# Kernel tuning notes

Measured on AMD Instinct MI355X. Metric: run time of the kernel, lower is better.

Reference implementation:

```python
import jax, jax.numpy as jnp
import numpy as np

N_NODES = 100000
N_EDGES = 3200000
N_GRAPHS = 64
IN_DIM, OUT_DIM = 16, 3


def _gcn_layer(x, src, dst, ew, W, b, n):
    # PyG GCNConv with edge_weight: transform first, then normalized propagate
    # with added self-loops (weight 1.0). deg_i = sum_{e: dst=i} w_e + 1.
    xw = x @ W  # [N, out]
    deg = jax.ops.segment_sum(ew, dst, num_segments=n) + 1.0  # [N]
    dinv = jax.lax.rsqrt(deg)
    norm = dinv[src] * ew * dinv[dst]  # [E]
    agg = jax.ops.segment_sum(xw[src] * norm[:, None], dst, num_segments=n)
    # self-loop contribution: dinv_i * 1.0 * dinv_i = 1/deg_i
    return agg + xw * (1.0 / deg)[:, None] + b


def setup_inputs() -> dict:
    key = jax.random.key(0)
    ks = jax.random.split(key, 16)
    glorot = lambda k, fi, fo: jax.random.normal(k, (fi, fo), jnp.float32) * jnp.sqrt(2.0 / (fi + fo))
    return {
        "x": jax.random.normal(ks[0], (N_NODES, IN_DIM), jnp.float32),
        "edge_index": jax.random.randint(ks[1], (2, N_EDGES), 0, N_NODES, jnp.int32),
        "edge_attr": jax.random.uniform(ks[2], (N_EDGES,), jnp.float32),
        "batch": jnp.sort(jax.random.randint(ks[3], (N_NODES,), 0, N_GRAPHS, jnp.int32)),
        "W1": glorot(ks[4], IN_DIM, 16), "b1": jnp.zeros((16,), jnp.float32),
        "W2": glorot(ks[5], 16, 64),     "b2": jnp.zeros((64,), jnp.float32),
        "W3": glorot(ks[6], 64, 256),    "b3": jnp.zeros((256,), jnp.float32),
        "L1": glorot(ks[7], 256, 128),   "c1": jnp.zeros((128,), jnp.float32),
        "L2": glorot(ks[8], 128, 64),    "c2": jnp.zeros((64,), jnp.float32),
        "L3": glorot(ks[9], 64, OUT_DIM), "c3": jnp.zeros((OUT_DIM,), jnp.float32),
    }


def reference(x, edge_index, edge_attr, batch, W1, b1, W2, b2, W3, b3, L1, c1, L2, c2, L3, c3):
    src, dst = edge_index[0], edge_index[1]
    h = jax.nn.silu(_gcn_layer(x, src, dst, edge_attr, W1, b1, N_NODES))
    h = jax.nn.silu(_gcn_layer(h, src, dst, edge_attr, W2, b2, N_NODES))
    h = jax.nn.silu(_gcn_layer(h, src, dst, edge_attr, W3, b3, N_NODES))
    # global mean pool per graph
    sums = jax.ops.segment_sum(h, batch, num_segments=N_GRAPHS)  # [G, 256]
    cnt = jax.ops.segment_sum(jnp.ones((N_NODES,), h.dtype), batch, num_segments=N_GRAPHS)
    pooled = sums / jnp.maximum(cnt, 1.0)[:, None]
    z = jax.nn.silu(pooled @ L1 + c1)
    z = jax.nn.silu(z @ L2 + c2)
    z = z @ L3 + c3
    return jnp.squeeze(z)
```

## Files before the change

kernel.cpp:

```cpp
#include <hip/hip_runtime.h>
#include <math.h>


#define NBH 256
#define POOL_C 8
#define X3T 32
#define CAP 10240

typedef _Float16 half8 __attribute__((ext_vector_type(8)));

__device__ __forceinline__ float silu_f(float v) { return v / (1.0f + expf(-v)); }
__device__ __forceinline__ void fma4(float4& a, float s, const float4& w) {
    a.x += s * w.x; a.y += s * w.y; a.z += s * w.z; a.w += s * w.w;
}

__global__ void k_init(const int* __restrict__ batch, int* __restrict__ bounds,
                       int* __restrict__ btotal, int N, int G) {
    int t = threadIdx.x;
    btotal[t] = 0;
    if (t > G) return;
    if (t == G) { bounds[G] = N; return; }
    int lo = 0, hi = N;
    while (lo < hi) { int m = (lo + hi) >> 1; if (batch[m] < t) lo = m + 1; else hi = m; }
    bounds[t] = lo;
}

__global__ __launch_bounds__(256) void k_bscatter(const int* __restrict__ src,
                                                  const int* __restrict__ dst,
                                                  const float* __restrict__ ew,
                                                  int* __restrict__ btotal,
                                                  int2* __restrict__ ebuf,
                                                  int E, int B, int ept) {
    __shared__ int hist[512];
    __shared__ int cur[512];
    int blk = blockIdx.x, t = threadIdx.x;
    for (int i = t; i < B; i += 256) hist[i] = 0;
    __syncthreads();
    int start = blk * 256 * ept;
    for (int j = 0; j < ept; j++) {
        int e = start + j * 256 + t;
        if (e < E) atomicAdd(&hist[dst[e] >> 8], 1);
    }
    __syncthreads();
    for (int b = t; b < B; b += 256)
        cur[b] = b * CAP + atomicAdd(&btotal[b], hist[b]);
    __syncthreads();
    for (int j = 0; j < ept; j++) {
        int e = start + j * 256 + t;
        if (e < E) {
            int d = dst[e];
            int b = d >> 8;
            int pos = atomicAdd(&cur[b], 1);
            if (pos < (b + 1) * CAP)
                ebuf[pos] = make_int2(src[e] | ((d & 255) << 24), __float_as_int(ew[e]));
        }
    }
}

__global__ __launch_bounds__(256) void k_bucket_csr(const int2* __restrict__ ebuf,
                                                    const int* __restrict__ btotal,
                                                    int2* __restrict__ csr,
                                                    unsigned int* __restrict__ offs,
                                                    float* __restrict__ dinv,
                                                    const float* __restrict__ x,
                                                    _Float16* __restrict__ xp,
                                                    int N) {
    __shared__ int ncnt[256];
    __shared__ int excl[256];
    __shared__ float wsum[256];
    int b = blockIdx.x, t = threadIdx.x;
    int base = b * CAP;
    int end = base + min(btotal[b], CAP);
    ncnt[t] = 0;
    wsum[t] = 0.0f;
    __syncthreads();
    for (int i = base + t; i < end; i += 256)
        atomicAdd(&ncnt[(unsigned)ebuf[i].x >> 24], 1);
    __syncthreads();
    int v = ncnt[t];
    excl[t] = v;
    __syncthreads();
#pragma unroll
    for (int o = 1; o < 256; o <<= 1) {
        int x2 = (t >= o) ? excl[t - o] : 0;
        __syncthreads();
        excl[t] += x2;
        __syncthreads();
    }
    int ex = excl[t] - v;
    int n = (b << 8) + t;
    if (n < N) offs[n] = (unsigned)(base + ex) | ((unsigned)v << 24);
    __syncthreads();
    ncnt[t] = base + ex;
    __syncthreads();
    for (int i = base + t; i < end; i += 256) {
        int2 ent = ebuf[i];
        int node = (unsigned)ent.x >> 24;
        int pos = atomicAdd(&ncnt[node], 1);
        csr[pos] = make_int2(ent.x & 0x00FFFFFF, ent.y);
        atomicAdd(&wsum[node], __int_as_float(ent.y));
    }
    __syncthreads();
    if (n < N) {
        float dv = 1.0f / sqrtf(1.0f + wsum[t]);
        dinv[n] = dv;
        const float4* xr = (const float4*)(x + (long long)n * 16);
        half8* xw = (half8*)(xp + (long long)n * 16);
#pragma unroll
        for (int j = 0; j < 2; j++) {
            float4 a = xr[2 * j], c = xr[2 * j + 1];
            half8 hv;
            hv[0] = (_Float16)(a.x * dv); hv[1] = (_Float16)(a.y * dv);
            hv[2] = (_Float16)(a.z * dv); hv[3] = (_Float16)(a.w * dv);
            hv[4] = (_Float16)(c.x * dv); hv[5] = (_Float16)(c.y * dv);
            hv[6] = (_Float16)(c.z * dv); hv[7] = (_Float16)(c.w * dv);
            xw[j] = hv;
        }
    }
}

__global__ __launch_bounds__(256) void k_gx1(const _Float16* __restrict__ h,
                                             const int2* __restrict__ csr,
                                             const unsigned int* __restrict__ offs,
                                             const float* __restrict__ dinv,
                                             const float* __restrict__ W,
                                             const float* __restrict__ b,
                                             _Float16* __restrict__ out, int N) {
    __shared__ float Ws[16 * 16];
    __shared__ float bs[16];
    if (threadIdx.x < 256) Ws[threadIdx.x] = W[threadIdx.x];
    if (threadIdx.x < 16) bs[threadIdx.x] = b[threadIdx.x];
    __syncthreads();
    int n = blockIdx.x * 4 + (threadIdx.x >> 6);
    n = __builtin_amdgcn_readfirstlane(n);
    if (n >= N) return;
    int lane = threadIdx.x & 63;
    int d = lane & 15, eg = lane >> 4;
    unsigned op = offs[n];
    int p0 = op & 0x00FFFFFF;
    int len = op >> 24;
    int qs = p0 + ((len * eg) >> 2);
    int qe = p0 + ((len * (eg + 1)) >> 2);
    float acc = 0.0f;
    int p = qs;
    for (; p + 7 < qe; p += 8) {
        int2 e0 = csr[p], e1 = csr[p + 1], e2 = csr[p + 2], e3 = csr[p + 3];
        int2 e4 = csr[p + 4], e5 = csr[p + 5], e6 = csr[p + 6], e7 = csr[p + 7];
        float v0 = (float)h[e0.x * 16 + d], v1 = (float)h[e1.x * 16 + d];
        float v2 = (float)h[e2.x * 16 + d], v3 = (float)h[e3.x * 16 + d];
        float v4 = (float)h[e4.x * 16 + d], v5 = (float)h[e5.x * 16 + d];
        float v6 = (float)h[e6.x * 16 + d], v7 = (float)h[e7.x * 16 + d];
        acc += __int_as_float(e0.y) * v0; acc += __int_as_float(e1.y) * v1;
        acc += __int_as_float(e2.y) * v2; acc += __int_as_float(e3.y) * v3;
        acc += __int_as_float(e4.y) * v4; acc += __int_as_float(e5.y) * v5;
        acc += __int_as_float(e6.y) * v6; acc += __int_as_float(e7.y) * v7;
    }
    if (p + 3 < qe) {
        int2 e0 = csr[p], e1 = csr[p + 1], e2 = csr[p + 2], e3 = csr[p + 3];
        float v0 = (float)h[e0.x * 16 + d], v1 = (float)h[e1.x * 16 + d];
        float v2 = (float)h[e2.x * 16 + d], v3 = (float)h[e3.x * 16 + d];
        acc += __int_as_float(e0.y) * v0; acc += __int_as_float(e1.y) * v1;
        acc += __int_as_float(e2.y) * v2; acc += __int_as_float(e3.y) * v3;
        p += 4;
    }
    if (p + 1 < qe) {
        int2 e0 = csr[p], e1 = csr[p + 1];
        acc += __int_as_float(e0.y) * (float)h[e0.x * 16 + d];
        acc += __int_as_float(e1.y) * (float)h[e1.x * 16 + d];
        p += 2;
    }
    if (p < qe) {
        int2 e0 = csr[p];
        acc += __int_as_float(e0.y) * (float)h[e0.x * 16 + d];
    }
    acc += __shfl_down(acc, 32, 64);
    acc += __shfl_down(acc, 16, 64);
    float dv = dinv[n];
    float yv = (acc + ((lane < 16) ? (float)h[n * 16 + lane] : 0.0f)) * dv;
    float o = bs[d];
#pragma unroll
    for (int k = 0; k < 16; k++) o += __shfl(yv, k, 64) * Ws[k * 16 + d];
    if (lane < 16) out[n * 16 + lane] = (_Float16)(silu_f(o) * dv);
}

__global__ __launch_bounds__(256) void k_gx2(const _Float16* __restrict__ h,
                                             const int2* __restrict__ csr,
                                             const unsigned int* __restrict__ offs,
                                             const float* __restrict__ dinv,
                                             const float* __restrict__ W,
                                             const float* __restrict__ b,
                                             _Float16* __restrict__ out, int N) {
    __shared__ float Ws[16 * 64];
    __shared__ float bs[64];
    for (int i = threadIdx.x; i < 16 * 64; i += 256) Ws[i] = W[i];
    if (threadIdx.x < 64) bs[threadIdx.x] = b[threadIdx.x];
    __syncthreads();
    int n = blockIdx.x * 4 + (threadIdx.x >> 6);
    n = __builtin_amdgcn_readfirstlane(n);
    if (n >= N) return;
    int lane = threadIdx.x & 63;
    int d = lane & 15, eg = lane >> 4;
    unsigned op = offs[n];
    int p0 = op & 0x00FFFFFF;
    int len = op >> 24;
    int qs = p0 + ((len * eg) >> 2);
    int qe = p0 + ((len * (eg + 1)) >> 2);
    float acc = 0.0f;
    int p = qs;
    for (; p + 7 < qe; p += 8) {
        int2 e0 = csr[p], e1 = csr[p + 1], e2 = csr[p + 2], e3 = csr[p + 3];
        int2 e4 = csr[p + 4], e5 = csr[p + 5], e6 = csr[p + 6], e7 = csr[p + 7];
        float v0 = (float)h[e0.x * 16 + d], v1 = (float)h[e1.x * 16 + d];
        float v2 = (float)h[e2.x * 16 + d], v3 = (float)h[e3.x * 16 + d];
        float v4 = (float)h[e4.x * 16 + d], v5 = (float)h[e5.x * 16 + d];
        float v6 = (float)h[e6.x * 16 + d], v7 = (float)h[e7.x * 16 + d];
        acc += __int_as_float(e0.y) * v0; acc += __int_as_float(e1.y) * v1;
        acc += __int_as_float(e2.y) * v2; acc += __int_as_float(e3.y) * v3;
        acc += __int_as_float(e4.y) * v4; acc += __int_as_float(e5.y) * v5;
        acc += __int_as_float(e6.y) * v6; acc += __int_as_float(e7.y) * v7;
    }
    if (p + 3 < qe) {
        int2 e0 = csr[p], e1 = csr[p + 1], e2 = csr[p + 2], e3 = csr[p + 3];
        float v0 = (float)h[e0.x * 16 + d], v1 = (float)h[e1.x * 16 + d];
        float v2 = (float)h[e2.x * 16 + d], v3 = (float)h[e3.x * 16 + d];
        acc += __int_as_float(e0.y) * v0; acc += __int_as_float(e1.y) * v1;
        acc += __int_as_float(e2.y) * v2; acc += __int_as_float(e3.y) * v3;
        p += 4;
    }
    if (p + 1 < qe) {
        int2 e0 = csr[p], e1 = csr[p + 1];
        acc += __int_as_float(e0.y) * (float)h[e0.x * 16 + d];
        acc += __int_as_float(e1.y) * (float)h[e1.x * 16 + d];
        p += 2;
    }
    if (p < qe) {
        int2 e0 = csr[p];
        acc += __int_as_float(e0.y) * (float)h[e0.x * 16 + d];
    }
    acc += __shfl_down(acc, 32, 64);
    acc += __shfl_down(acc, 16, 64);
    float dv = dinv[n];
    float yv = (acc + ((lane < 16) ? (float)h[n * 16 + lane] : 0.0f)) * dv;
    float o = bs[lane];
#pragma unroll
    for (int k = 0; k < 16; k++) o += __shfl(yv, k, 64) * Ws[k * 64 + lane];
    out[(long long)n * 64 + lane] = (_Float16)(silu_f(o) * dv);
}

__global__ __launch_bounds__(256) void k_gather64(const _Float16* __restrict__ h,
                                                  const int2* __restrict__ csr,
                                                  const unsigned int* __restrict__ offs,
                                                  const float* __restrict__ dinv,
                                                  float* __restrict__ y, int N) {
    int n = blockIdx.x * 4 + (threadIdx.x >> 6);
    n = __builtin_amdgcn_readfirstlane(n);
    if (n >= N) return;
    int lane = threadIdx.x & 63;
    unsigned op = offs[n];
    const int2* row = csr + (op & 0x00FFFFFF);
    int len = op >> 24;
    float acc = 0.0f;
    int j = 0;
    for (; j + 7 < len; j += 8) {
        int2 ee[8];
        float vv[8];
#pragma unroll
        for (int i = 0; i < 8; i++) ee[i] = row[j + i];
#pragma unroll
        for (int i = 0; i < 8; i++) vv[i] = (float)h[ee[i].x * 64 + lane];
#pragma unroll
        for (int i = 0; i < 8; i++) acc += __int_as_float(ee[i].y) * vv[i];
    }
    if (j + 3 < len) {
        int2 e0 = row[j], e1 = row[j + 1], e2 = row[j + 2], e3 = row[j + 3];
        float v0 = (float)h[e0.x * 64 + lane];
        float v1 = (float)h[e1.x * 64 + lane];
        float v2 = (float)h[e2.x * 64 + lane];
        float v3 = (float)h[e3.x * 64 + lane];
        acc += __int_as_float(e0.y) * v0;
        acc += __int_as_float(e1.y) * v1;
        acc += __int_as_float(e2.y) * v2;
        acc += __int_as_float(e3.y) * v3;
        j += 4;
    }
    for (; j < len; j++) {
        int2 e0 = row[j];
        acc += __int_as_float(e0.y) * (float)h[e0.x * 64 + lane];
    }
    y[n * 64 + lane] = (acc + (float)h[n * 64 + lane]) * dinv[n];
}

__global__ __launch_bounds__(256) void k_xform3pool(const float* __restrict__ y,
                                                    const float* __restrict__ W,
                                                    const float* __restrict__ b,
                                                    const int* __restrict__ bounds,
                                                    float* __restrict__ partial) {
    __shared__ float4 Ws[64 * 64];
    __shared__ float4 ys4[X3T * 16];
    __shared__ float4 red[3][64];
    for (int i = threadIdx.x; i < 64 * 64; i += 256) Ws[i] = ((const float4*)W)[i];
    int lane = threadIdx.x & 63;
    int wave = threadIdx.x >> 6;
    int g = blockIdx.x / POOL_C;
    int c = blockIdx.x % POOL_C;
    int s = bounds[g], e = bounds[g + 1];
    int len = e - s;
    int cs = s + (int)((long long)len * c / POOL_C);
    int ce = s + (int)((long long)len * (c + 1) / POOL_C);
    float4 bv = ((const float4*)b)[lane];
    float4 pacc = make_float4(0.f, 0.f, 0.f, 0.f);
    int nb = wave * 8;
    for (int base = cs; base < ce; base += X3T) {
        int tcnt = min(X3T, ce - base);
        __syncthreads();
        {
            const float4* ysrc = (const float4*)(y + (long long)base * 64);
            for (int i = threadIdx.x; i < tcnt * 16; i += 256) ys4[i] = ysrc[i];
        }
        __syncthreads();
        float4 acc[8];
#pragma unroll
        for (int i = 0; i < 8; i++) acc[i] = bv;
#pragma unroll 2
        for (int kq = 0; kq < 16; kq++) {
            float4 w0 = Ws[(4 * kq + 0) * 64 + lane];
            float4 w1 = Ws[(4 * kq + 1) * 64 + lane];
            float4 w2 = Ws[(4 * kq + 2) * 64 + lane];
            float4 w3 = Ws[(4 * kq + 3) * 64 + lane];
#pragma unroll
            for (int i = 0; i < 8; i++) {
                float4 yv = ys4[(nb + i) * 16 + kq];
                fma4(acc[i], yv.x, w0); fma4(acc[i], yv.y, w1);
                fma4(acc[i], yv.z, w2); fma4(acc[i], yv.w, w3);
            }
        }
#pragma unroll
        for (int i = 0; i < 8; i++) {
            if (base + nb + i < ce) {
                pacc.x += silu_f(acc[i].x); pacc.y += silu_f(acc[i].y);
                pacc.z += silu_f(acc[i].z); pacc.w += silu_f(acc[i].w);
            }
        }
    }
    __syncthreads();
    if (wave > 0) red[wave - 1][lane] = pacc;
    __syncthreads();
    if (wave == 0) {
        float4 r0 = red[0][lane], r1 = red[1][lane], r2 = red[2][lane];
        pacc.x += r0.x + r1.x + r2.x;
        pacc.y += r0.y + r1.y + r2.y;
        pacc.z += r0.z + r1.z + r2.z;
        pacc.w += r0.w + r1.w + r2.w;
        ((float4*)partial)[(long long)blockIdx.x * 64 + lane] = pacc;
    }
}

__global__ __launch_bounds__(256) void k_mlp(const float* __restrict__ partial,
                                             const int* __restrict__ bounds,
                                             const float* __restrict__ L1,
                                             const float* __restrict__ c1,
                                             const float* __restrict__ L2,
                                             const float* __restrict__ c2,
                                             const float* __restrict__ L3,
                                             const float* __restrict__ c3,
                                             float* __restrict__ out) {
    __shared__ float pooled[256];
    __shared__ float z1[128];
    __shared__ float z2[64];
    int g = blockIdx.x;
    int t = threadIdx.x;
    int cnt = bounds[g + 1] - bounds[g];
    float s = 0.0f;
    for (int c = 0; c < POOL_C; c++) s += partial[((long long)g * POOL_C + c) * 256 + t];
    pooled[t] = s / (float)(cnt > 0 ? cnt : 1);
    __syncthreads();
    if (t < 128) {
        float acc = c1[t];
        for (int k = 0; k < 256; k++) acc += pooled[k] * L1[k * 128 + t];
        z1[t] = silu_f(acc);
    }
    __syncthreads();
    if (t < 64) {
        float acc = c2[t];
        for (int k = 0; k < 128; k++) acc += z1[k] * L2[k * 64 + t];
        z2[t] = silu_f(acc);
    }
    __syncthreads();
    if (t < 3) {
        float acc = c3[t];
        for (int k = 0; k < 64; k++) acc += z2[k] * L3[k * 3 + t];
        out[g * 3 + t] = acc;
    }
}

extern "C" void kernel_launch(void* const* d_in, const int* in_sizes, int n_in,
                              void* d_out, int out_size, void* d_ws, size_t ws_size,
                              hipStream_t stream) {
    const float* x     = (const float*)d_in[0];
    const int*   ei    = (const int*)d_in[1];
    const float* ea    = (const float*)d_in[2];
    const int*   batch = (const int*)d_in[3];
    const float* W1 = (const float*)d_in[4];
    const float* b1 = (const float*)d_in[5];
    const float* W2 = (const float*)d_in[6];
    const float* b2 = (const float*)d_in[7];
    const float* W3 = (const float*)d_in[8];
    const float* b3 = (const float*)d_in[9];
    const float* L1 = (const float*)d_in[10];
    const float* c1 = (const float*)d_in[11];
    const float* L2 = (const float*)d_in[12];
    const float* c2 = (const float*)d_in[13];
    const float* L3 = (const float*)d_in[14];
    const float* c3 = (const float*)d_in[15];
    float* out = (float*)d_out;

    const int N = in_sizes[0] / 16;
    const int E = in_sizes[2];
    const int G = out_size / 3;
    const int* src = ei;
    const int* dst = ei + E;
    const int B = (N + 255) >> 8;
    const int ept = (E + NBH * 256 - 1) / (NBH * 256);

    char* ws = (char*)d_ws;
    size_t off = 0;
    auto alloc = [&](size_t bytes) -> void* {
        void* p = (void*)(ws + off);
        off += (bytes + 255) & ~(size_t)255;
        return p;
    };
    float*        dinv    = (float*)alloc((size_t)N * 4);
    unsigned int* offs    = (unsigned int*)alloc((size_t)N * 4);
    int*          btotal  = (int*)  alloc(512 * 4);
    int*          bounds  = (int*)  alloc((size_t)(G + 1) * 4);
    int2*         ebuf    = (int2*) alloc((size_t)B * CAP * 8);
    int2*         csr     = (int2*) alloc((size_t)B * CAP * 8);
    _Float16*     xp      = (_Float16*)alloc((size_t)N * 16 * 2);
    _Float16*     h1s     = (_Float16*)alloc((size_t)N * 16 * 2);
    _Float16*     h2s     = (_Float16*)alloc((size_t)N * 64 * 2);
    float*        y64     = (float*)alloc((size_t)N * 64 * 4);
    float*        partial = (float*)alloc((size_t)G * POOL_C * 256 * 4);
    (void)ws_size;

    k_init<<<1, 512, 0, stream>>>(batch, bounds, btotal, N, G);
    k_bscatter<<<NBH, 256, 0, stream>>>(src, dst, ea, btotal, ebuf, E, B, ept);
    k_bucket_csr<<<B, 256, 0, stream>>>(ebuf, btotal, csr, offs, dinv, x, xp, N);

    k_gx1<<<(N + 3) / 4, 256, 0, stream>>>(xp, csr, offs, dinv, W1, b1, h1s, N);

    k_gx2<<<(N + 3) / 4, 256, 0, stream>>>(h1s, csr, offs, dinv, W2, b2, h2s, N);

    k_gather64<<<(N + 3) / 4, 256, 0, stream>>>(h2s, csr, offs, dinv, y64, N);
    k_xform3pool<<<G * POOL_C, 256, 0, stream>>>(y64, W3, b3, bounds, partial);

    k_mlp<<<G, 256, 0, stream>>>(partial, bounds, L1, c1, L2, c2, L3, c3, out);
}
```

Before: 477.3 us.

## Use FP16 MFMA for layer-3 transform and pool, store y64 in half

```diff
diff --git a/kernel.cpp b/kernel.cpp
--- a/kernel.cpp
+++ b/kernel.cpp
@@ -4,15 +4,12 @@
 
 #define NBH 256
 #define POOL_C 8
-#define X3T 32
 #define CAP 10240
 
 typedef _Float16 half8 __attribute__((ext_vector_type(8)));
+typedef float f32x4 __attribute__((ext_vector_type(4)));
 
 __device__ __forceinline__ float silu_f(float v) { return v / (1.0f + expf(-v)); }
-__device__ __forceinline__ void fma4(float4& a, float s, const float4& w) {
-    a.x += s * w.x; a.y += s * w.y; a.z += s * w.z; a.w += s * w.w;
-}
 
 __global__ void k_init(const int* __restrict__ batch, int* __restrict__ bounds,
                        int* __restrict__ btotal, int N, int G) {
@@ -23,6 +20,12 @@
     int lo = 0, hi = N;
     while (lo < hi) { int m = (lo + hi) >> 1; if (batch[m] < t) lo = m + 1; else hi = m; }
     bounds[t] = lo;
+}
+
+__global__ __launch_bounds__(256) void k_cvtW3(const float* __restrict__ W,
+                                               _Float16* __restrict__ Wh, int n) {
+    int i = blockIdx.x * 256 + threadIdx.x;
+    if (i < n) Wh[i] = (_Float16)W[i];
 }
 
 __global__ __launch_bounds__(256) void k_bscatter(const int* __restrict__ src,
@@ -251,7 +254,7 @@
                                                   const int2* __restrict__ csr,
                                                   const unsigned int* __restrict__ offs,
                                                   const float* __restrict__ dinv,
-                                                  float* __restrict__ y, int N) {
+                                                  _Float16* __restrict__ y, int N) {
     int n = blockIdx.x * 4 + (threadIdx.x >> 6);
     n = __builtin_amdgcn_readfirstlane(n);
     if (n >= N) return;
@@ -287,18 +290,15 @@
         int2 e0 = row[j];
         acc += __int_as_float(e0.y) * (float)h[e0.x * 64 + lane];
     }
-    y[n * 64 + lane] = (acc + (float)h[n * 64 + lane]) * dinv[n];
-}
-
-__global__ __launch_bounds__(256) void k_xform3pool(const float* __restrict__ y,
-                                                    const float* __restrict__ W,
+    y[n * 64 + lane] = (_Float16)((acc + (float)h[n * 64 + lane]) * dinv[n]);
+}
+
+__global__ __launch_bounds__(256) void k_xform3pool(const _Float16* __restrict__ y,
+                                                    const _Float16* __restrict__ Wh,
                                                     const float* __restrict__ b,
                                                     const int* __restrict__ bounds,
-                                                    float* __restrict__ partial) {
-    __shared__ float4 Ws[64 * 64];
-    __shared__ float4 ys4[X3T * 16];
-    __shared__ float4 red[3][64];
-    for (int i = threadIdx.x; i < 64 * 64; i += 256) Ws[i] = ((const float4*)W)[i];
+                                                    float* __restrict__ partial,
+                                                    int N) {
     int lane = threadIdx.x & 63;
     int wave = threadIdx.x >> 6;
     int g = blockIdx.x / POOL_C;
@@ -307,51 +307,55 @@
     int len = e - s;
     int cs = s + (int)((long long)len * c / POOL_C);
     int ce = s + (int)((long long)len * (c + 1) / POOL_C);
-    float4 bv = ((const float4*)b)[lane];
-    float4 pacc = make_float4(0.f, 0.f, 0.f, 0.f);
-    int nb = wave * 8;
-    for (int base = cs; base < ce; base += X3T) {
-        int tcnt = min(X3T, ce - base);
-        __syncthreads();
-        {
-            const float4* ysrc = (const float4*)(y + (long long)base * 64);
-            for (int i = threadIdx.x; i < tcnt * 16; i += 256) ys4[i] = ysrc[i];
+    int lg = lane >> 4;
+    int lr = lane & 15;
+
+    half8 bf[4][2];
+#pragma unroll
+    for (int t = 0; t < 4; t++) {
+        int col = (wave * 4 + t) * 16 + lr;
+#pragma unroll
+        for (int s2 = 0; s2 < 2; s2++) {
+            half8 v;
+#pragma unroll
+            for (int j = 0; j < 8; j++)
+                v[j] = Wh[(s2 * 32 + lg * 8 + j) * 256 + col];
+            bf[t][s2] = v;
         }
-        __syncthreads();
-        float4 acc[8];
-#pragma unroll
-        for (int i = 0; i < 8; i++) acc[i] = bv;
-#pragma unroll 2
-        for (int kq = 0; kq < 16; kq++) {
-            float4 w0 = Ws[(4 * kq + 0) * 64 + lane];
-            float4 w1 = Ws[(4 * kq + 1) * 64 + lane];
-            float4 w2 = Ws[(4 * kq + 2) * 64 + lane];
-            float4 w3 = Ws[(4 * kq + 3) * 64 + lane];
-#pragma unroll
-            for (int i = 0; i < 8; i++) {
-                float4 yv = ys4[(nb + i) * 16 + kq];
-                fma4(acc[i], yv.x, w0); fma4(acc[i], yv.y, w1);
-                fma4(acc[i], yv.z, w2); fma4(acc[i], yv.w, w3);
+    }
+    float bias[4];
+#pragma unroll
+    for (int t = 0; t < 4; t++) bias[t] = b[(wave * 4 + t) * 16 + lr];
+
+    float pacc[4] = {0.f, 0.f, 0.f, 0.f};
+
+    for (int base = cs; base < ce; base += 16) {
+        int node = base + lr;
+        int cn = node < N ? node : N - 1;
+        const half8* arow = (const half8*)(y + (long long)cn * 64);
+        half8 a0 = arow[lg];
+        half8 a1 = arow[4 + lg];
+#pragma unroll
+        for (int t = 0; t < 4; t++) {
+            f32x4 acc = {0.f, 0.f, 0.f, 0.f};
+            acc = __builtin_amdgcn_mfma_f32_16x16x32_f16(a0, bf[t][0], acc, 0, 0, 0);
+            acc = __builtin_amdgcn_mfma_f32_16x16x32_f16(a1, bf[t][1], acc, 0, 0, 0);
+#pragma unroll
+            for (int r = 0; r < 4; r++) {
+                int nrow = base + lg * 4 + r;
+                if (nrow < ce) pacc[t] += silu_f(acc[r] + bias[t]);
             }
         }
-#pragma unroll
-        for (int i = 0; i < 8; i++) {
-            if (base + nb + i < ce) {
-                pacc.x += silu_f(acc[i].x); pacc.y += silu_f(acc[i].y);
-                pacc.z += silu_f(acc[i].z); pacc.w += silu_f(acc[i].w);
-            }
-        }
-    }
-    __syncthreads();
-    if (wave > 0) red[wave - 1][lane] = pacc;
-    __syncthreads();
-    if (wave == 0) {
-        float4 r0 = red[0][lane], r1 = red[1][lane], r2 = red[2][lane];
-        pacc.x += r0.x + r1.x + r2.x;
-        pacc.y += r0.y + r1.y + r2.y;
-        pacc.z += r0.z + r1.z + r2.z;
-        pacc.w += r0.w + r1.w + r2.w;
-        ((float4*)partial)[(long long)blockIdx.x * 64 + lane] = pacc;
+    }
+#pragma unroll
+    for (int t = 0; t < 4; t++) {
+        pacc[t] += __shfl_xor(pacc[t], 16, 64);
+        pacc[t] += __shfl_xor(pacc[t], 32, 64);
+    }
+    if (lane < 16) {
+        float* pr = partial + (long long)blockIdx.x * 256 + wave * 64;
+#pragma unroll
+        for (int t = 0; t < 4; t++) pr[t * 16 + lane] = pacc[t];
     }
 }
 
@@ -438,11 +442,13 @@
     _Float16*     xp      = (_Float16*)alloc((size_t)N * 16 * 2);
     _Float16*     h1s     = (_Float16*)alloc((size_t)N * 16 * 2);
     _Float16*     h2s     = (_Float16*)alloc((size_t)N * 64 * 2);
-    float*        y64     = (float*)alloc((size_t)N * 64 * 4);
+    _Float16*     y64     = (_Float16*)alloc((size_t)N * 64 * 2);
+    _Float16*     W3h     = (_Float16*)alloc((size_t)64 * 256 * 2);
     float*        partial = (float*)alloc((size_t)G * POOL_C * 256 * 4);
     (void)ws_size;
 
     k_init<<<1, 512, 0, stream>>>(batch, bounds, btotal, N, G);
+    k_cvtW3<<<64, 256, 0, stream>>>(W3, W3h, 64 * 256);
     k_bscatter<<<NBH, 256, 0, stream>>>(src, dst, ea, btotal, ebuf, E, B, ept);
     k_bucket_csr<<<B, 256, 0, stream>>>(ebuf, btotal, csr, offs, dinv, x, xp, N);
 
@@ -451,7 +457,7 @@
     k_gx2<<<(N + 3) / 4, 256, 0, stream>>>(h1s, csr, offs, dinv, W2, b2, h2s, N);
 
     k_gather64<<<(N + 3) / 4, 256, 0, stream>>>(h2s, csr, offs, dinv, y64, N);
-    k_xform3pool<<<G * POOL_C, 256, 0, stream>>>(y64, W3, b3, bounds, partial);
+    k_xform3pool<<<G * POOL_C, 256, 0, stream>>>(y64, W3h, b3, bounds, partial, N);
 
     k_mlp<<<G, 256, 0, stream>>>(partial, bounds, L1, c1, L2, c2, L3, c3, out);
 }
```

Result: faster. 433.6 us (-9.2%).
